# Optimization experiments

Hardware: AMD Instinct MI355X
Metric: run time of the kernel (lower is better)

Reference implementation:

```python
import jax, jax.numpy as jnp
import numpy as np

B, S, H = 4, 512, 1024
E, K, I = 8, 2, 2048

def setup_inputs() -> dict:
    key = jax.random.key(0)
    k1, k2, k3, k4, k5 = jax.random.split(key, 5)
    scale_h = 1.0 / np.sqrt(H)
    scale_i = 1.0 / np.sqrt(I)
    return {
        "hidden_states": jax.random.normal(k1, (B, S, H), dtype=jnp.float32),
        "router_w": jax.random.normal(k2, (E, H), dtype=jnp.float32) * scale_h,
        "w_gate": jax.random.normal(k3, (E, H, I), dtype=jnp.float32) * scale_h,
        "w_up": jax.random.normal(k4, (E, H, I), dtype=jnp.float32) * scale_h,
        "w_down": jax.random.normal(k5, (E, I, H), dtype=jnp.float32) * scale_i,
    }

def reference(hidden_states, router_w, w_gate, w_up, w_down):
    b, s, h = hidden_states.shape
    x = hidden_states.reshape(-1, h)              # [T, H] tokens
    T = x.shape[0]

    # ---- RouterTopK: fp32 linear -> softmax over all experts -> top-k ----
    router_logits = x.astype(jnp.float32) @ router_w.T          # [T, E]
    probs = jax.nn.softmax(router_logits, axis=-1)               # [T, E]
    top_vals, top_idx = jax.lax.top_k(probs, K)                  # [T, K]

    # normalize_top_k_affinities (norm_topk_prob=True)
    top_vals = top_vals / jnp.sum(top_vals, axis=-1, keepdims=True)

    # scatter normalized affinities into a dense [T, E] combine matrix
    aff = jnp.zeros((T, E), dtype=x.dtype).at[jnp.arange(T)[:, None], top_idx].set(top_vals.astype(x.dtype))

    # ---- ExpertMLPs: GLU (swiglu) per expert, combine weighted by affinity ----
    # Dense-per-expert computation; non-selected experts contribute 0 via aff.
    gate = jnp.einsum('th,ehi->eti', x, w_gate)                  # [E, T, I]
    up = jnp.einsum('th,ehi->eti', x, w_up)                      # [E, T, I]
    act = jax.nn.silu(gate) * up                                 # [E, T, I]
    expert_out = jnp.einsum('eti,eih->eth', act, w_down)         # [E, T, H]
    out = jnp.einsum('eth,te->th', expert_out, aff)              # [T, H]

    # _reduce_output: all-reduce over TP/world group -> identity single-device
    return out.reshape(b, s, h)
```

## Files before the change

kernel.cpp:

```cpp
#include <hip/hip_runtime.h>
#include <hip/hip_bf16.h>

#define T_TOK 2048
#define H_DIM 1024
#define E_N   8
#define I_DIM 2048
#define GW    4096

#define NT_MAX 40
#define SLOTS  5120

typedef unsigned short u16;
typedef unsigned int   u32;
typedef __bf16 bf16_t;
typedef bf16_t bf16x8 __attribute__((ext_vector_type(8)));
typedef u16    u16x8  __attribute__((ext_vector_type(8)));
typedef u16    u16x4  __attribute__((ext_vector_type(4)));
typedef float  f32x16 __attribute__((ext_vector_type(16)));

#define MFMA32 __builtin_amdgcn_mfma_f32_32x32x16_bf16

__device__ __forceinline__ u16 bfbits(float f) {
    bf16_t b = (bf16_t)f;
    return __builtin_bit_cast(u16, b);
}
__device__ __forceinline__ float bf2f(u16 u) {
    u32 x = ((u32)u) << 16;
    return __builtin_bit_cast(float, x);
}

__device__ __forceinline__ void gload_lds16(const void* g, void* l) {
    __builtin_amdgcn_global_load_lds(
        (const __attribute__((address_space(1))) void*)g,
        (__attribute__((address_space(3))) void*)l, 16, 0, 0);
}

__device__ __forceinline__ int tile_off(int n, int kb) {
    return n * 64 + ((kb ^ ((n >> 1) & 7)) << 3);
}
__device__ __forceinline__ int a_off(int row, int kslot) {
    return row * 64 + ((kslot ^ (row & 7)) << 3);
}

__global__ __launch_bounds__(256) void router_k(
    const float* __restrict__ x, const float* __restrict__ rw,
    int* __restrict__ cnt, int* __restrict__ tok,
    int4* __restrict__ invA, float2* __restrict__ invW,
    u16* __restrict__ xbf)
{
    int wid = threadIdx.x >> 6, lane = threadIdx.x & 63;
    int t = blockIdx.x * 4 + wid;
    const float* xr = x + (size_t)t * H_DIM;
    u16* xbr = xbf + (size_t)t * H_DIM;

    float acc[E_N];
#pragma unroll
    for (int e = 0; e < E_N; e++) acc[e] = 0.f;
    for (int j = 0; j < H_DIM / 64; j++) {
        float xv = xr[lane + 64 * j];
        xbr[lane + 64 * j] = bfbits(xv);
#pragma unroll
        for (int e = 0; e < E_N; e++)
            acc[e] += xv * rw[e * H_DIM + lane + 64 * j];
    }
#pragma unroll
    for (int e = 0; e < E_N; e++) {
        float v = acc[e];
        for (int off = 32; off; off >>= 1) v += __shfl_xor(v, off);
        acc[e] = v;
    }
    if (lane == 0) {
        int i0 = 0; float m0 = acc[0];
#pragma unroll
        for (int e = 1; e < E_N; e++) if (acc[e] > m0) { m0 = acc[e]; i0 = e; }
        int i1 = -1; float m1 = -INFINITY;
#pragma unroll
        for (int e = 0; e < E_N; e++) if (e != i0 && acc[e] > m1) { m1 = acc[e]; i1 = e; }
        float w0 = 1.f / (1.f + expf(m1 - m0));
        float w1 = 1.f - w0;
        int p0 = atomicAdd(&cnt[i0], 1);
        tok[i0 * T_TOK + p0] = t;
        int p1 = atomicAdd(&cnt[i1], 1);
        tok[i1 * T_TOK + p1] = t;
        invA[t] = make_int4(i0, p0, i1, p1);
        invW[t] = make_float2(w0, w1);
    }
}

__global__ void prefix_k(const int* __restrict__ cnt, int* __restrict__ offs_pad,
                         int* __restrict__ tile_e, int* __restrict__ tile_row0,
                         int* __restrict__ ntiles)
{
    if (threadIdx.x == 0) {
        int s = 0, nt = 0;
        for (int e = 0; e < E_N; e++) {
            offs_pad[e] = s;
            int c = cnt[e];
            int t = (c + 127) >> 7;
            for (int i = 0; i < t; i++) { tile_e[nt] = e; tile_row0[nt] = i * 128; nt++; }
            s += t * 128;
        }
        offs_pad[E_N] = s;
        *ntiles = nt;
    }
}

__global__ __launch_bounds__(256, 2) void gu_k(
    const u16* __restrict__ xbf, const float* __restrict__ wg, const float* __restrict__ wu,
    const int* __restrict__ cnt, const int* __restrict__ offs_pad,
    const int* __restrict__ tile_e, const int* __restrict__ tile_row0,
    const int* __restrict__ ntiles, const int* __restrict__ tok,
    u16* __restrict__ gbuf)
{
    int q = gridDim.x >> 3;
    int phys = blockIdx.x;
    int logical = (phys & 7) * q + (phys >> 3);
    int tb = logical % NT_MAX;
    int p  = logical / NT_MAX;
    if (tb >= *ntiles) return;
    int e = tile_e[tb], row0 = tile_row0[tb];
    int cntE = cnt[e];
    int slot0 = offs_pad[e] + row0;
    int n0 = p * 128;
    int mat  = n0 >> 11;
    int coln = n0 & 2047;

    __shared__ u16 AS[2][8192], BS[2][8192];

    int tid = threadIdx.x;
    int lane = tid & 63, wid = tid >> 6;
    int wm = wid >> 1, wn = wid & 1;
    int l31 = lane & 31, lh = lane >> 5;

    const u16* asrc[4];
#pragma unroll
    for (int i = 0; i < 4; i++) {
        int row = (wid * 4 + i) * 8 + (lane >> 3);
        int rc = (row0 + row < cntE) ? (row0 + row) : (cntE - 1);
        asrc[i] = xbf + (size_t)tok[e * T_TOK + rc] * H_DIM
                  + (((lane & 7) ^ ((lane >> 3) & 7)) << 3);
    }
    int s0 = wid * 2048;

    int bn = tid & 127;
    int khalf = tid >> 7;
    const float* wsrc = (mat ? wu : wg) + (size_t)e * H_DIM * I_DIM + coln + bn;

    float v0[32], v1[32];

#define BLOAD(vs, t) { \
    _Pragma("unroll") \
    for (int j = 0; j < 32; j++) \
        vs[j] = wsrc[(size_t)((t) * 64 + khalf * 32 + j) * I_DIM]; }

#define BWRITE(vs, nbuf) { \
    _Pragma("unroll") \
    for (int jb = 0; jb < 4; jb++) { \
        u16x8 pk; \
        _Pragma("unroll") \
        for (int jj = 0; jj < 8; jj++) pk[jj] = bfbits(vs[jb * 8 + jj]); \
        *reinterpret_cast<u16x8*>(&BS[nbuf][tile_off(bn, khalf * 4 + jb)]) = pk; } }

#define ASTAGE(nbuf, t) { \
    _Pragma("unroll") \
    for (int i = 0; i < 4; i++) \
        gload_lds16(asrc[i] + (size_t)(t) * 64, &AS[nbuf][s0 + i * 512]); }

    f32x16 acc[2][2];
#pragma unroll
    for (int a = 0; a < 2; a++)
#pragma unroll
        for (int b = 0; b < 2; b++) acc[a][b] = (f32x16)0.f;

#define CLUSTER(bufi) { \
    _Pragma("unroll") \
    for (int ks = 0; ks < 4; ks++) { \
        bf16x8 af[2], bfr[2]; \
        _Pragma("unroll") \
        for (int mf = 0; mf < 2; mf++) \
            af[mf] = *reinterpret_cast<const bf16x8*>(&AS[bufi][a_off(wm * 64 + mf * 32 + l31, ks * 2 + lh)]); \
        _Pragma("unroll") \
        for (int nf = 0; nf < 2; nf++) \
            bfr[nf] = *reinterpret_cast<const bf16x8*>(&BS[bufi][tile_off(wn * 64 + nf * 32 + l31, ks * 2 + lh)]); \
        _Pragma("unroll") \
        for (int mf = 0; mf < 2; mf++) \
            _Pragma("unroll") \
            for (int nf = 0; nf < 2; nf++) \
                acc[mf][nf] = MFMA32(af[mf], bfr[nf], acc[mf][nf], 0, 0, 0); } }

    ASTAGE(0, 0);
    __builtin_amdgcn_sched_barrier(0);
    BLOAD(v0, 0);
    __builtin_amdgcn_sched_barrier(0);
    BLOAD(v1, 1);
    __builtin_amdgcn_sched_barrier(0);
    BWRITE(v0, 0);
    __builtin_amdgcn_sched_barrier(0);
    asm volatile("s_waitcnt vmcnt(0) lgkmcnt(0)" ::: "memory");
    __builtin_amdgcn_s_barrier();
    __builtin_amdgcn_sched_barrier(0);

    for (int t2 = 0; t2 < 16; t2 += 2) {
        if (t2 + 1 < 16) ASTAGE(1, t2 + 1);
        CLUSTER(0);
        __builtin_amdgcn_sched_barrier(0);
        if (t2 + 1 < 16) BWRITE(v1, 1);
        __builtin_amdgcn_sched_barrier(0);
        if (t2 + 2 < 16) {
            BLOAD(v0, t2 + 2);
            __builtin_amdgcn_sched_barrier(0);
            asm volatile("s_waitcnt vmcnt(32) lgkmcnt(0)" ::: "memory");
        } else {
            asm volatile("s_waitcnt vmcnt(0) lgkmcnt(0)" ::: "memory");
        }
        __builtin_amdgcn_s_barrier();
        __builtin_amdgcn_sched_barrier(0);

        {
            int t = t2 + 1;
            if (t + 1 < 16) ASTAGE(0, t + 1);
            CLUSTER(1);
            __builtin_amdgcn_sched_barrier(0);
            if (t + 1 < 16) {
                BWRITE(v0, 0);
                __builtin_amdgcn_sched_barrier(0);
                if (t + 2 < 16) {
                    BLOAD(v1, t + 2);
                    __builtin_amdgcn_sched_barrier(0);
                    asm volatile("s_waitcnt vmcnt(32) lgkmcnt(0)" ::: "memory");
                } else {
                    asm volatile("s_waitcnt vmcnt(0) lgkmcnt(0)" ::: "memory");
                }
                __builtin_amdgcn_s_barrier();
                __builtin_amdgcn_sched_barrier(0);
            }
        }
    }
#undef BLOAD
#undef BWRITE
#undef ASTAGE
#undef CLUSTER

#pragma unroll
    for (int mf = 0; mf < 2; mf++)
#pragma unroll
        for (int nf = 0; nf < 2; nf++) {
            int col = n0 + wn * 64 + nf * 32 + l31;
#pragma unroll
            for (int r = 0; r < 16; r++) {
                int rl = wm * 64 + mf * 32 + (r & 3) + 8 * (r >> 2) + 4 * lh;
                gbuf[(size_t)(slot0 + rl) * GW + col] = bfbits(acc[mf][nf][r]);
            }
        }
}

__global__ __launch_bounds__(256) void act_k(const u16* __restrict__ gbuf,
                                             u16* __restrict__ act)
{
    int s = blockIdx.x;
    int i = threadIdx.x * 8;
    u16x8 g8 = *reinterpret_cast<const u16x8*>(&gbuf[(size_t)s * GW + i]);
    u16x8 u8 = *reinterpret_cast<const u16x8*>(&gbuf[(size_t)s * GW + 2048 + i]);
    u16x8 o;
#pragma unroll
    for (int j = 0; j < 8; j++) {
        float g = bf2f(g8[j]);
        float u = bf2f(u8[j]);
        o[j] = bfbits(g / (1.f + expf(-g)) * u);
    }
    *reinterpret_cast<u16x8*>(&act[(size_t)s * I_DIM + i]) = o;
}

__global__ __launch_bounds__(256, 2) void down_k(
    const u16* __restrict__ act, const float* __restrict__ wd,
    const int* __restrict__ cnt, const int* __restrict__ offs_pad,
    const int* __restrict__ tile_e, const int* __restrict__ tile_row0,
    const int* __restrict__ ntiles, const int* __restrict__ tok,
    u16* __restrict__ dbuf)
{
    int q = gridDim.x >> 3;
    int phys = blockIdx.x;
    int logical = (phys & 7) * q + (phys >> 3);
    int tb = logical % NT_MAX;
    int rest = logical / NT_MAX;
    int p  = rest & 7;
    int kh = rest >> 3;
    if (tb >= *ntiles) return;
    int e = tile_e[tb], row0 = tile_row0[tb];
    int slot0 = offs_pad[e] + row0;
    int h0 = p * 128;

    __shared__ u16 AS[2][8192], BS[2][8192];

    int tid = threadIdx.x;
    int lane = tid & 63, wid = tid >> 6;
    int wm = wid >> 1, wn = wid & 1;
    int l31 = lane & 31, lh = lane >> 5;

    const u16* asrc[4];
#pragma unroll
    for (int i = 0; i < 4; i++) {
        int row = (wid * 4 + i) * 8 + (lane >> 3);
        asrc[i] = act + (size_t)(slot0 + row) * I_DIM + kh * 1024
                  + (((lane & 7) ^ ((lane >> 3) & 7)) << 3);
    }
    int s0 = wid * 2048;

    int bn = tid & 127;
    int khalf = tid >> 7;
    const float* dsrc = wd + ((size_t)e * I_DIM + kh * 1024) * H_DIM + h0 + bn;

    float v0[32], v1[32];

#define BLOAD(vs, t) { \
    _Pragma("unroll") \
    for (int j = 0; j < 32; j++) \
        vs[j] = dsrc[(size_t)((t) * 64 + khalf * 32 + j) * H_DIM]; }

#define BWRITE(vs, nbuf) { \
    _Pragma("unroll") \
    for (int jb = 0; jb < 4; jb++) { \
        u16x8 pk; \
        _Pragma("unroll") \
        for (int jj = 0; jj < 8; jj++) pk[jj] = bfbits(vs[jb * 8 + jj]); \
        *reinterpret_cast<u16x8*>(&BS[nbuf][tile_off(bn, khalf * 4 + jb)]) = pk; } }

#define ASTAGE(nbuf, t) { \
    _Pragma("unroll") \
    for (int i = 0; i < 4; i++) \
        gload_lds16(asrc[i] + (size_t)(t) * 64, &AS[nbuf][s0 + i * 512]); }

    f32x16 acc[2][2];
#pragma unroll
    for (int a = 0; a < 2; a++)
#pragma unroll
        for (int b = 0; b < 2; b++) acc[a][b] = (f32x16)0.f;

#define CLUSTER(bufi) { \
    _Pragma("unroll") \
    for (int ks = 0; ks < 4; ks++) { \
        bf16x8 af[2], bfr[2]; \
        _Pragma("unroll") \
        for (int mf = 0; mf < 2; mf++) \
            af[mf] = *reinterpret_cast<const bf16x8*>(&AS[bufi][a_off(wm * 64 + mf * 32 + l31, ks * 2 + lh)]); \
        _Pragma("unroll") \
        for (int nf = 0; nf < 2; nf++) \
            bfr[nf] = *reinterpret_cast<const bf16x8*>(&BS[bufi][tile_off(wn * 64 + nf * 32 + l31, ks * 2 + lh)]); \
        _Pragma("unroll") \
        for (int mf = 0; mf < 2; mf++) \
            _Pragma("unroll") \
            for (int nf = 0; nf < 2; nf++) \
                acc[mf][nf] = MFMA32(af[mf], bfr[nf], acc[mf][nf], 0, 0, 0); } }

    ASTAGE(0, 0);
    __builtin_amdgcn_sched_barrier(0);
    BLOAD(v0, 0);
    __builtin_amdgcn_sched_barrier(0);
    BLOAD(v1, 1);
    __builtin_amdgcn_sched_barrier(0);
    BWRITE(v0, 0);
    __builtin_amdgcn_sched_barrier(0);
    asm volatile("s_waitcnt vmcnt(0) lgkmcnt(0)" ::: "memory");
    __builtin_amdgcn_s_barrier();
    __builtin_amdgcn_sched_barrier(0);

    for (int t2 = 0; t2 < 16; t2 += 2) {
        if (t2 + 1 < 16) ASTAGE(1, t2 + 1);
        CLUSTER(0);
        __builtin_amdgcn_sched_barrier(0);
        if (t2 + 1 < 16) BWRITE(v1, 1);
        __builtin_amdgcn_sched_barrier(0);
        if (t2 + 2 < 16) {
            BLOAD(v0, t2 + 2);
            __builtin_amdgcn_sched_barrier(0);
            asm volatile("s_waitcnt vmcnt(32) lgkmcnt(0)" ::: "memory");
        } else {
            asm volatile("s_waitcnt vmcnt(0) lgkmcnt(0)" ::: "memory");
        }
        __builtin_amdgcn_s_barrier();
        __builtin_amdgcn_sched_barrier(0);

        {
            int t = t2 + 1;
            if (t + 1 < 16) ASTAGE(0, t + 1);
            CLUSTER(1);
            __builtin_amdgcn_sched_barrier(0);
            if (t + 1 < 16) {
                BWRITE(v0, 0);
                __builtin_amdgcn_sched_barrier(0);
                if (t + 2 < 16) {
                    BLOAD(v1, t + 2);
                    __builtin_amdgcn_sched_barrier(0);
                    asm volatile("s_waitcnt vmcnt(32) lgkmcnt(0)" ::: "memory");
                } else {
                    asm volatile("s_waitcnt vmcnt(0) lgkmcnt(0)" ::: "memory");
                }
                __builtin_amdgcn_s_barrier();
                __builtin_amdgcn_sched_barrier(0);
            }
        }
    }
#undef BLOAD
#undef BWRITE
#undef ASTAGE
#undef CLUSTER

#pragma unroll
    for (int mf = 0; mf < 2; mf++)
#pragma unroll
        for (int nf = 0; nf < 2; nf++) {
            int col = h0 + wn * 64 + nf * 32 + l31;
#pragma unroll
            for (int r = 0; r < 16; r++) {
                int rl = wm * 64 + mf * 32 + (r & 3) + 8 * (r >> 2) + 4 * lh;
                dbuf[(size_t)(kh * SLOTS + slot0 + rl) * H_DIM + col] = bfbits(acc[mf][nf][r]);
            }
        }
}

__global__ __launch_bounds__(256) void gather_k(
    const u16* __restrict__ dbuf, const int4* __restrict__ invA,
    const float2* __restrict__ invW, const int* __restrict__ offs_pad,
    float* __restrict__ out)
{
    int t = blockIdx.x;
    int h = threadIdx.x * 4;
    int4 ia = invA[t];
    float2 w = invW[t];
    int s0 = offs_pad[ia.x] + ia.y;
    int s1 = offs_pad[ia.z] + ia.w;

    u16x4 a0 = *reinterpret_cast<const u16x4*>(&dbuf[(size_t)s0 * H_DIM + h]);
    u16x4 a1 = *reinterpret_cast<const u16x4*>(&dbuf[(size_t)(SLOTS + s0) * H_DIM + h]);
    u16x4 b0 = *reinterpret_cast<const u16x4*>(&dbuf[(size_t)s1 * H_DIM + h]);
    u16x4 b1 = *reinterpret_cast<const u16x4*>(&dbuf[(size_t)(SLOTS + s1) * H_DIM + h]);

    float4 o;
    float* op = &o.x;
#pragma unroll
    for (int j = 0; j < 4; j++)
        op[j] = w.x * (bf2f(a0[j]) + bf2f(a1[j])) + w.y * (bf2f(b0[j]) + bf2f(b1[j]));
    *reinterpret_cast<float4*>(&out[(size_t)t * H_DIM + h]) = o;
}

extern "C" void kernel_launch(void* const* d_in, const int* in_sizes, int n_in,
                              void* d_out, int out_size, void* d_ws, size_t ws_size,
                              hipStream_t stream)
{
    const float* x  = (const float*)d_in[0];
    const float* rw = (const float*)d_in[1];
    const float* wg = (const float*)d_in[2];
    const float* wu = (const float*)d_in[3];
    const float* wd = (const float*)d_in[4];
    float* out = (float*)d_out;

    char* ws = (char*)d_ws;
    int*    cnt       = (int*)(ws);
    int*    ntiles    = (int*)(ws + 32);
    int*    offs_pad  = (int*)(ws + 64);
    int*    tile_e    = (int*)(ws + 256);
    int*    tile_row0 = (int*)(ws + 512);
    int*    tok       = (int*)(ws + 64 * 1024);
    int4*   invA      = (int4*)(ws + 160 * 1024);
    float2* invW      = (float2*)(ws + 200 * 1024);
    u16*    xbf       = (u16*)(ws + 256 * 1024);
    u16*    act       = (u16*)(ws + 5ull * 1024 * 1024);
    u16*    gbuf      = (u16*)(ws + 26ull * 1024 * 1024);
    u16*    dbuf      = (u16*)(ws + 67ull * 1024 * 1024);

    size_t need = 88ull * 1024 * 1024;
    if (ws_size < need) return;

    hipMemsetAsync(cnt, 0, 32, stream);

    router_k<<<T_TOK / 4, 256, 0, stream>>>(x, rw, cnt, tok, invA, invW, xbf);
    prefix_k<<<1, 64, 0, stream>>>(cnt, offs_pad, tile_e, tile_row0, ntiles);
    gu_k<<<NT_MAX * (GW / 128), 256, 0, stream>>>(
        xbf, wg, wu, cnt, offs_pad, tile_e, tile_row0, ntiles, tok, gbuf);
    act_k<<<SLOTS, 256, 0, stream>>>(gbuf, act);
    down_k<<<NT_MAX * (H_DIM / 128) * 2, 256, 0, stream>>>(
        act, wd, cnt, offs_pad, tile_e, tile_row0, ntiles, tok, dbuf);
    gather_k<<<T_TOK, 256, 0, stream>>>(dbuf, invA, invW, offs_pad, out);
}
```

Measured before the change: 231.7 us.

## Single-buffer B tile and register prefetch to raise GEMM occupancy; vectorize router

```diff
diff --git a/kernel.cpp b/kernel.cpp
--- a/kernel.cpp
+++ b/kernel.cpp
@@ -56,12 +56,18 @@
     float acc[E_N];
 #pragma unroll
     for (int e = 0; e < E_N; e++) acc[e] = 0.f;
-    for (int j = 0; j < H_DIM / 64; j++) {
-        float xv = xr[lane + 64 * j];
-        xbr[lane + 64 * j] = bfbits(xv);
-#pragma unroll
-        for (int e = 0; e < E_N; e++)
-            acc[e] += xv * rw[e * H_DIM + lane + 64 * j];
+#pragma unroll
+    for (int j = 0; j < H_DIM / 256; j++) {
+        int o = lane * 4 + j * 256;
+        float4 xv = *reinterpret_cast<const float4*>(xr + o);
+        u16x4 p;
+        p[0] = bfbits(xv.x); p[1] = bfbits(xv.y); p[2] = bfbits(xv.z); p[3] = bfbits(xv.w);
+        *reinterpret_cast<u16x4*>(xbr + o) = p;
+#pragma unroll
+        for (int e = 0; e < E_N; e++) {
+            float4 wv = *reinterpret_cast<const float4*>(rw + e * H_DIM + o);
+            acc[e] += xv.x * wv.x + xv.y * wv.y + xv.z * wv.z + xv.w * wv.w;
+        }
     }
 #pragma unroll
     for (int e = 0; e < E_N; e++) {
@@ -105,7 +111,7 @@
     }
 }
 
-__global__ __launch_bounds__(256, 2) void gu_k(
+__global__ __launch_bounds__(256, 3) void gu_k(
     const u16* __restrict__ xbf, const float* __restrict__ wg, const float* __restrict__ wu,
     const int* __restrict__ cnt, const int* __restrict__ offs_pad,
     const int* __restrict__ tile_e, const int* __restrict__ tile_row0,
@@ -125,7 +131,7 @@
     int mat  = n0 >> 11;
     int coln = n0 & 2047;
 
-    __shared__ u16 AS[2][8192], BS[2][8192];
+    __shared__ u16 AS[2][8192], BS[8192];
 
     int tid = threadIdx.x;
     int lane = tid & 63, wid = tid >> 6;
@@ -146,20 +152,20 @@
     int khalf = tid >> 7;
     const float* wsrc = (mat ? wu : wg) + (size_t)e * H_DIM * I_DIM + coln + bn;
 
-    float v0[32], v1[32];
-
-#define BLOAD(vs, t) { \
+    float v[32];
+
+#define BLOAD(t) { \
     _Pragma("unroll") \
     for (int j = 0; j < 32; j++) \
-        vs[j] = wsrc[(size_t)((t) * 64 + khalf * 32 + j) * I_DIM]; }
-
-#define BWRITE(vs, nbuf) { \
+        v[j] = wsrc[(size_t)((t) * 64 + khalf * 32 + j) * I_DIM]; }
+
+#define BWRITE() { \
     _Pragma("unroll") \
     for (int jb = 0; jb < 4; jb++) { \
         u16x8 pk; \
         _Pragma("unroll") \
-        for (int jj = 0; jj < 8; jj++) pk[jj] = bfbits(vs[jb * 8 + jj]); \
-        *reinterpret_cast<u16x8*>(&BS[nbuf][tile_off(bn, khalf * 4 + jb)]) = pk; } }
+        for (int jj = 0; jj < 8; jj++) pk[jj] = bfbits(v[jb * 8 + jj]); \
+        *reinterpret_cast<u16x8*>(&BS[tile_off(bn, khalf * 4 + jb)]) = pk; } }
 
 #define ASTAGE(nbuf, t) { \
     _Pragma("unroll") \
@@ -181,7 +187,7 @@
             af[mf] = *reinterpret_cast<const bf16x8*>(&AS[bufi][a_off(wm * 64 + mf * 32 + l31, ks * 2 + lh)]); \
         _Pragma("unroll") \
         for (int nf = 0; nf < 2; nf++) \
-            bfr[nf] = *reinterpret_cast<const bf16x8*>(&BS[bufi][tile_off(wn * 64 + nf * 32 + l31, ks * 2 + lh)]); \
+            bfr[nf] = *reinterpret_cast<const bf16x8*>(&BS[tile_off(wn * 64 + nf * 32 + l31, ks * 2 + lh)]); \
         _Pragma("unroll") \
         for (int mf = 0; mf < 2; mf++) \
             _Pragma("unroll") \
@@ -190,50 +196,33 @@
 
     ASTAGE(0, 0);
     __builtin_amdgcn_sched_barrier(0);
-    BLOAD(v0, 0);
-    __builtin_amdgcn_sched_barrier(0);
-    BLOAD(v1, 1);
-    __builtin_amdgcn_sched_barrier(0);
-    BWRITE(v0, 0);
+    BLOAD(0);
+    __builtin_amdgcn_sched_barrier(0);
+    BWRITE();
     __builtin_amdgcn_sched_barrier(0);
     asm volatile("s_waitcnt vmcnt(0) lgkmcnt(0)" ::: "memory");
     __builtin_amdgcn_s_barrier();
     __builtin_amdgcn_sched_barrier(0);
 
-    for (int t2 = 0; t2 < 16; t2 += 2) {
-        if (t2 + 1 < 16) ASTAGE(1, t2 + 1);
-        CLUSTER(0);
+    for (int t = 0; t < 16; t++) {
+        int abuf = t & 1;
+        bool more = (t + 1) < 16;
+        if (more) {
+            ASTAGE(abuf ^ 1, t + 1);
+            __builtin_amdgcn_sched_barrier(0);
+            BLOAD(t + 1);
+            __builtin_amdgcn_sched_barrier(0);
+        }
+        CLUSTER(abuf);
         __builtin_amdgcn_sched_barrier(0);
-        if (t2 + 1 < 16) BWRITE(v1, 1);
-        __builtin_amdgcn_sched_barrier(0);
-        if (t2 + 2 < 16) {
-            BLOAD(v0, t2 + 2);
-            __builtin_amdgcn_sched_barrier(0);
-            asm volatile("s_waitcnt vmcnt(32) lgkmcnt(0)" ::: "memory");
-        } else {
+        if (more) {
+            __builtin_amdgcn_s_barrier();
+            __builtin_amdgcn_sched_barrier(0);
+            BWRITE();
+            __builtin_amdgcn_sched_barrier(0);
             asm volatile("s_waitcnt vmcnt(0) lgkmcnt(0)" ::: "memory");
-        }
-        __builtin_amdgcn_s_barrier();
-        __builtin_amdgcn_sched_barrier(0);
-
-        {
-            int t = t2 + 1;
-            if (t + 1 < 16) ASTAGE(0, t + 1);
-            CLUSTER(1);
-            __builtin_amdgcn_sched_barrier(0);
-            if (t + 1 < 16) {
-                BWRITE(v0, 0);
-                __builtin_amdgcn_sched_barrier(0);
-                if (t + 2 < 16) {
-                    BLOAD(v1, t + 2);
-                    __builtin_amdgcn_sched_barrier(0);
-                    asm volatile("s_waitcnt vmcnt(32) lgkmcnt(0)" ::: "memory");
-                } else {
-                    asm volatile("s_waitcnt vmcnt(0) lgkmcnt(0)" ::: "memory");
-                }
-                __builtin_amdgcn_s_barrier();
-                __builtin_amdgcn_sched_barrier(0);
-            }
+            __builtin_amdgcn_s_barrier();
+            __builtin_amdgcn_sched_barrier(0);
         }
     }
 #undef BLOAD
@@ -271,7 +260,7 @@
     *reinterpret_cast<u16x8*>(&act[(size_t)s * I_DIM + i]) = o;
 }
 
-__global__ __launch_bounds__(256, 2) void down_k(
+__global__ __launch_bounds__(256, 3) void down_k(
     const u16* __restrict__ act, const float* __restrict__ wd,
     const int* __restrict__ cnt, const int* __restrict__ offs_pad,
     const int* __restrict__ tile_e, const int* __restrict__ tile_row0,
@@ -290,7 +279,7 @@
     int slot0 = offs_pad[e] + row0;
     int h0 = p * 128;
 
-    __shared__ u16 AS[2][8192], BS[2][8192];
+    __shared__ u16 AS[2][8192], BS[8192];
 
     int tid = threadIdx.x;
     int lane = tid & 63, wid = tid >> 6;
@@ -310,20 +299,20 @@
     int khalf = tid >> 7;
     const float* dsrc = wd + ((size_t)e * I_DIM + kh * 1024) * H_DIM + h0 + bn;
 
-    float v0[32], v1[32];
-
-#define BLOAD(vs, t) { \
+    float v[32];
+
+#define BLOAD(t) { \
     _Pragma("unroll") \
     for (int j = 0; j < 32; j++) \
-        vs[j] = dsrc[(size_t)((t) * 64 + khalf * 32 + j) * H_DIM]; }
-
-#define BWRITE(vs, nbuf) { \
+        v[j] = dsrc[(size_t)((t) * 64 + khalf * 32 + j) * H_DIM]; }
+
+#define BWRITE() { \
     _Pragma("unroll") \
     for (int jb = 0; jb < 4; jb++) { \
         u16x8 pk; \
         _Pragma("unroll") \
-        for (int jj = 0; jj < 8; jj++) pk[jj] = bfbits(vs[jb * 8 + jj]); \
-        *reinterpret_cast<u16x8*>(&BS[nbuf][tile_off(bn, khalf * 4 + jb)]) = pk; } }
+        for (int jj = 0; jj < 8; jj++) pk[jj] = bfbits(v[jb * 8 + jj]); \
+        *reinterpret_cast<u16x8*>(&BS[tile_off(bn, khalf * 4 + jb)]) = pk; } }
 
 #define ASTAGE(nbuf, t) { \
     _Pragma("unroll") \
@@ -345,7 +334,7 @@
             af[mf] = *reinterpret_cast<const bf16x8*>(&AS[bufi][a_off(wm * 64 + mf * 32 + l31, ks * 2 + lh)]); \
         _Pragma("unroll") \
         for (int nf = 0; nf < 2; nf++) \
-            bfr[nf] = *reinterpret_cast<const bf16x8*>(&BS[bufi][tile_off(wn * 64 + nf * 32 + l31, ks * 2 + lh)]); \
+            bfr[nf] = *reinterpret_cast<const bf16x8*>(&BS[tile_off(wn * 64 + nf * 32 + l31, ks * 2 + lh)]); \
         _Pragma("unroll") \
         for (int mf = 0; mf < 2; mf++) \
             _Pragma("unroll") \
@@ -354,50 +343,33 @@
 
     ASTAGE(0, 0);
     __builtin_amdgcn_sched_barrier(0);
-    BLOAD(v0, 0);
-    __builtin_amdgcn_sched_barrier(0);
-    BLOAD(v1, 1);
-    __builtin_amdgcn_sched_barrier(0);
-    BWRITE(v0, 0);
+    BLOAD(0);
+    __builtin_amdgcn_sched_barrier(0);
+    BWRITE();
     __builtin_amdgcn_sched_barrier(0);
     asm volatile("s_waitcnt vmcnt(0) lgkmcnt(0)" ::: "memory");
     __builtin_amdgcn_s_barrier();
     __builtin_amdgcn_sched_barrier(0);
 
-    for (int t2 = 0; t2 < 16; t2 += 2) {
-        if (t2 + 1 < 16) ASTAGE(1, t2 + 1);
-        CLUSTER(0);
+    for (int t = 0; t < 16; t++) {
+        int abuf = t & 1;
+        bool more = (t + 1) < 16;
+        if (more) {
+            ASTAGE(abuf ^ 1, t + 1);
+            __builtin_amdgcn_sched_barrier(0);
+            BLOAD(t + 1);
+            __builtin_amdgcn_sched_barrier(0);
+        }
+        CLUSTER(abuf);
         __builtin_amdgcn_sched_barrier(0);
-        if (t2 + 1 < 16) BWRITE(v1, 1);
-        __builtin_amdgcn_sched_barrier(0);
-        if (t2 + 2 < 16) {
-            BLOAD(v0, t2 + 2);
-            __builtin_amdgcn_sched_barrier(0);
-            asm volatile("s_waitcnt vmcnt(32) lgkmcnt(0)" ::: "memory");
-        } else {
+        if (more) {
+            __builtin_amdgcn_s_barrier();
+            __builtin_amdgcn_sched_barrier(0);
+            BWRITE();
+            __builtin_amdgcn_sched_barrier(0);
             asm volatile("s_waitcnt vmcnt(0) lgkmcnt(0)" ::: "memory");
-        }
-        __builtin_amdgcn_s_barrier();
-        __builtin_amdgcn_sched_barrier(0);
-
-        {
-            int t = t2 + 1;
-            if (t + 1 < 16) ASTAGE(0, t + 1);
-            CLUSTER(1);
-            __builtin_amdgcn_sched_barrier(0);
-            if (t + 1 < 16) {
-                BWRITE(v0, 0);
-                __builtin_amdgcn_sched_barrier(0);
-                if (t + 2 < 16) {
-                    BLOAD(v1, t + 2);
-                    __builtin_amdgcn_sched_barrier(0);
-                    asm volatile("s_waitcnt vmcnt(32) lgkmcnt(0)" ::: "memory");
-                } else {
-                    asm volatile("s_waitcnt vmcnt(0) lgkmcnt(0)" ::: "memory");
-                }
-                __builtin_amdgcn_s_barrier();
-                __builtin_amdgcn_sched_barrier(0);
-            }
+            __builtin_amdgcn_s_barrier();
+            __builtin_amdgcn_sched_barrier(0);
         }
     }
 #undef BLOAD
```

Result: faster. 206.9 us (-10.7%).
